# Kernel optimization log

Measured on AMD Instinct MI355X. Metric: run time of the kernel, lower is better.

## Reference

```python
import jax, jax.numpy as jnp
import numpy as np
import math

N_HEADS = 16


def setup_inputs() -> dict:
    key = jax.random.key(0)
    ks = jax.random.split(key, 5)
    B, S, E = 2, 2048, 1024
    scale = 1.0 / math.sqrt(E)
    return {
        "x": jax.random.normal(ks[0], (B, S, E), dtype=jnp.float32),
        "w_in": jax.random.normal(ks[1], (3 * E, E), dtype=jnp.float32) * scale,
        "b_in": jax.random.normal(ks[2], (3 * E,), dtype=jnp.float32) * 0.01,
        "w_out": jax.random.normal(ks[3], (E, E), dtype=jnp.float32) * scale,
        "b_out": jax.random.normal(ks[4], (E,), dtype=jnp.float32) * 0.01,
    }


def reference(x, w_in, b_in, w_out, b_out):
    B, S, E = x.shape
    H = N_HEADS
    d = E // H
    # fused QKV projection: [B,S,3E]
    qkv = x @ w_in.T + b_in
    q, k, v = jnp.split(qkv, 3, axis=-1)
    # [B,S,E] -> [B,H,S,d]
    q = q.reshape(B, S, H, d).transpose(0, 2, 1, 3)
    k = k.reshape(B, S, H, d).transpose(0, 2, 1, 3)
    v = v.reshape(B, S, H, d).transpose(0, 2, 1, 3)
    # scores [B,H,S,S], scaled by 1/sqrt(d_head) (no causal mask: casual_mask=False)
    scores = jnp.einsum("bhqd,bhkd->bhqk", q, k) / jnp.sqrt(jnp.float32(d)).astype(x.dtype)
    w = jax.nn.softmax(scores, axis=-1)
    # attention output [B,H,S,d] -> [B,S,E]
    out = jnp.einsum("bhqk,bhkd->bhqd", w, v)
    out = out.transpose(0, 2, 1, 3).reshape(B, S, E)
    return out @ w_out.T + b_out
```

## Files before the change

### kernel.cpp

```cpp
#include <hip/hip_runtime.h>
#include <cstdint>


typedef __bf16 bf16x8 __attribute__((ext_vector_type(8)));
typedef short s16x4 __attribute__((ext_vector_type(4)));
typedef float f32x4 __attribute__((ext_vector_type(4)));

__device__ __forceinline__ unsigned short f32_to_bf16_rne(float f) {
    unsigned int u = __builtin_bit_cast(unsigned int, f);
    u += 0x7FFF + ((u >> 16) & 1);
    return (unsigned short)(u >> 16);
}

__device__ __forceinline__ unsigned int pack_bf16_trunc(float a, float b) {
    unsigned int ua = __builtin_bit_cast(unsigned int, a);
    unsigned int ub = __builtin_bit_cast(unsigned int, b);
    return __builtin_amdgcn_perm(ub, ua, 0x07060302u);
}

__device__ __forceinline__ void gload16(const void* g, void* l) {
    __builtin_amdgcn_global_load_lds(
        (const __attribute__((address_space(1))) unsigned int*)g,
        (__attribute__((address_space(3))) unsigned int*)l, 16, 0, 0);
}

__global__ void cvt_all(const float* __restrict__ x, const float* __restrict__ wi,
                        const float* __restrict__ wo, unsigned short* __restrict__ xb,
                        unsigned short* __restrict__ wib, unsigned short* __restrict__ wob) {
    int i = blockIdx.x * blockDim.x + threadIdx.x;
    const float* src; unsigned short* dst; int off;
    if (i < 1048576)            { src = x;  dst = xb;  off = i; }
    else if (i < 1048576 + 786432) { src = wi; dst = wib; off = i - 1048576; }
    else                        { src = wo; dst = wob; off = i - (1048576 + 786432); }
    float4 v = ((const float4*)src)[off];
    ushort4 o;
    o.x = f32_to_bf16_rne(v.x); o.y = f32_to_bf16_rne(v.y);
    o.z = f32_to_bf16_rne(v.z); o.w = f32_to_bf16_rne(v.w);
    ((ushort4*)dst)[off] = o;
}

__launch_bounds__(256)
__global__ void gemm_qkv(const unsigned short* __restrict__ X,
                         const unsigned short* __restrict__ W,
                         const float* __restrict__ bias,
                         unsigned short* __restrict__ Qp,
                         unsigned short* __restrict__ Kp,
                         unsigned short* __restrict__ Vt) {
    __shared__ __align__(16) unsigned short As[128 * 64];
    __shared__ __align__(16) unsigned short Bs[128 * 64];
    const int t = threadIdx.x;
    const int w = t >> 6, lane = t & 63, quad = lane >> 4, l16 = lane & 15;
    const int wm = (w >> 1) * 64, wn = (w & 1) * 64;
    const int m0 = blockIdx.y * 128, n0 = blockIdx.x * 128;

    f32x4 acc[4][4] = {};

    for (int kt = 0; kt < 1024; kt += 64) {
        __syncthreads();
#pragma unroll
        for (int i = 0; i < 4; ++i) {
            int c = t + 256 * i;
            int r = c >> 3, cc = (c & 7) * 8;
            gload16(&X[(m0 + r) * 1024 + kt + cc], &As[c * 8]);
            gload16(&W[(n0 + r) * 1024 + kt + cc], &Bs[c * 8]);
        }
        __syncthreads();
#pragma unroll
        for (int ks = 0; ks < 2; ++ks) {
            bf16x8 af[4], bw[4];
#pragma unroll
            for (int mi = 0; mi < 4; ++mi)
                af[mi] = *(const bf16x8*)&As[(wm + mi * 16 + l16) * 64 + ks * 32 + quad * 8];
#pragma unroll
            for (int ni = 0; ni < 4; ++ni)
                bw[ni] = *(const bf16x8*)&Bs[(wn + ni * 16 + l16) * 64 + ks * 32 + quad * 8];
#pragma unroll
            for (int mi = 0; mi < 4; ++mi)
#pragma unroll
                for (int ni = 0; ni < 4; ++ni)
                    acc[mi][ni] = __builtin_amdgcn_mfma_f32_16x16x32_bf16(af[mi], bw[ni], acc[mi][ni], 0, 0, 0);
        }
    }

    const float QSCALE = 0.125f * 1.44269504089f;
#pragma unroll
    for (int mi = 0; mi < 4; ++mi) {
#pragma unroll
        for (int ni = 0; ni < 4; ++ni) {
            int col = n0 + wn + ni * 16 + l16;
            float bv = bias[col];
            int which = col >> 10;
            int hc = col & 1023;
            int h = hc >> 6, d = hc & 63;
            int row0 = m0 + wm + mi * 16 + quad * 4;
            int b = row0 >> 11, s0 = row0 & 2047;
            int bh = b * 16 + h;
            if (which == 2) {
                ushort4 pk;
                pk.x = f32_to_bf16_rne(acc[mi][ni][0] + bv);
                pk.y = f32_to_bf16_rne(acc[mi][ni][1] + bv);
                pk.z = f32_to_bf16_rne(acc[mi][ni][2] + bv);
                pk.w = f32_to_bf16_rne(acc[mi][ni][3] + bv);
                *(ushort4*)&Vt[(bh * 64 + d) * 2048 + s0] = pk;
            } else if (which == 0) {
#pragma unroll
                for (int r = 0; r < 4; ++r)
                    Qp[(bh * 2048 + s0 + r) * 64 + d] =
                        f32_to_bf16_rne((acc[mi][ni][r] + bv) * QSCALE);
            } else {
#pragma unroll
                for (int r = 0; r < 4; ++r)
                    Kp[(bh * 2048 + s0 + r) * 64 + d] = f32_to_bf16_rne(acc[mi][ni][r] + bv);
            }
        }
    }
}

__launch_bounds__(128, 2)
__global__ void attn(const unsigned short* __restrict__ Qp, const unsigned short* __restrict__ Kp,
                     const unsigned short* __restrict__ Vt, unsigned short* __restrict__ A2) {
    __shared__ __align__(16) unsigned short Ks[2][64 * 64];
    __shared__ __align__(16) unsigned short Vs[2][64 * 64];
    const int t = threadIdx.x, w = t >> 6, lane = t & 63, quad = lane >> 4, l16 = lane & 15;
    const int bh = blockIdx.x;
    const int qb = blockIdx.y;
    const unsigned short* Qh = Qp + bh * (2048 * 64);
    const unsigned short* Kh = Kp + bh * (2048 * 64);
    const unsigned short* Vh = Vt + bh * (64 * 2048);

    bf16x8 qf[2][2];
#pragma unroll
    for (int nq = 0; nq < 2; ++nq)
#pragma unroll
        for (int ks = 0; ks < 2; ++ks) {
            int row = qb * 64 + w * 32 + nq * 16 + l16;
            qf[nq][ks] = *(const bf16x8*)&Qh[row * 64 + ks * 32 + quad * 8];
        }

    f32x4 o_acc[4][2] = {};
    float l_lane[2] = {0.f, 0.f};

#pragma unroll
    for (int i = 0; i < 4; ++i) {
        int c = t + 128 * i;
        int r = c >> 3, sc = ((c & 7) ^ (r & 7)) << 3;
        gload16(&Kh[r * 64 + sc], &Ks[0][c * 8]);
        gload16(&Vh[r * 2048 + sc], &Vs[0][c * 8]);
    }

    int cur = 0;
    for (int it = 0; it < 32; ++it) {
        __syncthreads();
        if (it != 31) {
            int ktn = (it + 1) * 64;
#pragma unroll
            for (int i = 0; i < 4; ++i) {
                int c = t + 128 * i;
                int r = c >> 3, sc = ((c & 7) ^ (r & 7)) << 3;
                gload16(&Kh[(ktn + r) * 64 + sc], &Ks[cur ^ 1][c * 8]);
                gload16(&Vh[r * 2048 + ktn + sc], &Vs[cur ^ 1][c * 8]);
            }
        }
        const unsigned short* Kc = Ks[cur];
        const unsigned short* Vc = Vs[cur];

        f32x4 s_acc[4][2] = {};
#pragma unroll
        for (int ks = 0; ks < 2; ++ks)
#pragma unroll
            for (int mi = 0; mi < 4; ++mi) {
                bf16x8 kf = *(const bf16x8*)&Kc[(mi * 16 + l16) * 64 +
                                                (((ks * 4 + quad) ^ (l16 & 7)) << 3)];
#pragma unroll
                for (int nq = 0; nq < 2; ++nq)
                    s_acc[mi][nq] = __builtin_amdgcn_mfma_f32_16x16x32_bf16(kf, qf[nq][ks], s_acc[mi][nq], 0, 0, 0);
            }

        s16x4 bq[4][2];
#pragma unroll
        for (int nq = 0; nq < 2; ++nq) {
            float rsum = 0.f;
#pragma unroll
            for (int mi = 0; mi < 4; ++mi) {
                float p0 = __builtin_amdgcn_exp2f(s_acc[mi][nq][0]);
                float p1 = __builtin_amdgcn_exp2f(s_acc[mi][nq][1]);
                float p2 = __builtin_amdgcn_exp2f(s_acc[mi][nq][2]);
                float p3 = __builtin_amdgcn_exp2f(s_acc[mi][nq][3]);
                rsum += (p0 + p1) + (p2 + p3);
                uint2 pk;
                pk.x = pack_bf16_trunc(p0, p1);
                pk.y = pack_bf16_trunc(p2, p3);
                bq[mi][nq] = __builtin_bit_cast(s16x4, pk);
            }
            l_lane[nq] += rsum;
        }

#pragma unroll
        for (int dm = 0; dm < 4; ++dm)
#pragma unroll
            for (int kt4 = 0; kt4 < 4; ++kt4) {
                int ch = (kt4 * 2 + (quad >> 1)) ^ (l16 & 7);
                s16x4 av = __builtin_bit_cast(s16x4,
                    *(const uint2*)&Vc[(dm * 16 + l16) * 64 + (ch << 3) + (quad & 1) * 4]);
#pragma unroll
                for (int nq = 0; nq < 2; ++nq)
                    o_acc[dm][nq] = __builtin_amdgcn_mfma_f32_16x16x16bf16_1k(av, bq[kt4][nq], o_acc[dm][nq], 0, 0, 0);
            }
        cur ^= 1;
    }

    const int b = bh >> 4, h = bh & 15;
#pragma unroll
    for (int nq = 0; nq < 2; ++nq) {
        float l = l_lane[nq];
        l += __shfl_xor(l, 16);
        l += __shfl_xor(l, 32);
        float rl = 1.0f / l;
        int s = qb * 64 + w * 32 + nq * 16 + l16;
        int tok = b * 2048 + s;
#pragma unroll
        for (int dm = 0; dm < 4; ++dm) {
            ushort4 o;
            o.x = f32_to_bf16_rne(o_acc[dm][nq][0] * rl);
            o.y = f32_to_bf16_rne(o_acc[dm][nq][1] * rl);
            o.z = f32_to_bf16_rne(o_acc[dm][nq][2] * rl);
            o.w = f32_to_bf16_rne(o_acc[dm][nq][3] * rl);
            *(ushort4*)&A2[tok * 1024 + h * 64 + dm * 16 + quad * 4] = o;
        }
    }
}

__launch_bounds__(256)
__global__ void gemm_out_k(const unsigned short* __restrict__ A, const unsigned short* __restrict__ W,
                           const float* __restrict__ bias, float* __restrict__ out) {
    __shared__ __align__(16) unsigned short As[128 * 64];
    __shared__ __align__(16) unsigned short Bs[64 * 64];
    const int t = threadIdx.x;
    const int w = t >> 6, lane = t & 63, quad = lane >> 4, l16 = lane & 15;
    const int wm = (w >> 1) * 64, wn = (w & 1) * 32;
    const int m0 = blockIdx.y * 128, n0 = blockIdx.x * 64;

    f32x4 acc[4][2] = {};

    for (int kt = 0; kt < 1024; kt += 64) {
        __syncthreads();
#pragma unroll
        for (int i = 0; i < 4; ++i) {
            int c = t + 256 * i;
            int r = c >> 3, cc = (c & 7) * 8;
            gload16(&A[(m0 + r) * 1024 + kt + cc], &As[c * 8]);
        }
#pragma unroll
        for (int i = 0; i < 2; ++i) {
            int c = t + 256 * i;
            int r = c >> 3, cc = (c & 7) * 8;
            gload16(&W[(n0 + r) * 1024 + kt + cc], &Bs[c * 8]);
        }
        __syncthreads();
#pragma unroll
        for (int ks = 0; ks < 2; ++ks) {
            bf16x8 af[4], bw[2];
#pragma unroll
            for (int mi = 0; mi < 4; ++mi)
                af[mi] = *(const bf16x8*)&As[(wm + mi * 16 + l16) * 64 + ks * 32 + quad * 8];
#pragma unroll
            for (int ni = 0; ni < 2; ++ni)
                bw[ni] = *(const bf16x8*)&Bs[(wn + ni * 16 + l16) * 64 + ks * 32 + quad * 8];
#pragma unroll
            for (int mi = 0; mi < 4; ++mi)
#pragma unroll
                for (int ni = 0; ni < 2; ++ni)
                    acc[mi][ni] = __builtin_amdgcn_mfma_f32_16x16x32_bf16(af[mi], bw[ni], acc[mi][ni], 0, 0, 0);
        }
    }

#pragma unroll
    for (int mi = 0; mi < 4; ++mi)
#pragma unroll
        for (int ni = 0; ni < 2; ++ni) {
            int col = n0 + wn + ni * 16 + l16;
            float bv = bias[col];
#pragma unroll
            for (int r = 0; r < 4; ++r) {
                int row = m0 + wm + mi * 16 + quad * 4 + r;
                out[row * 1024 + col] = acc[mi][ni][r] + bv;
            }
        }
}

extern "C" void kernel_launch(void* const* d_in, const int* in_sizes, int n_in,
                              void* d_out, int out_size, void* d_ws, size_t ws_size,
                              hipStream_t stream) {
    const float* x     = (const float*)d_in[0];
    const float* w_in  = (const float*)d_in[1];
    const float* b_in  = (const float*)d_in[2];
    const float* w_out = (const float*)d_in[3];
    const float* b_out = (const float*)d_in[4];
    float* out = (float*)d_out;

    char* ws = (char*)d_ws;
    unsigned short* xb  = (unsigned short*)(ws);
    unsigned short* wib = (unsigned short*)(ws + 8388608);
    unsigned short* wob = (unsigned short*)(ws + 14680064);
    unsigned short* Qp  = (unsigned short*)(ws + 16777216);
    unsigned short* Kp  = (unsigned short*)(ws + 25165824);
    unsigned short* Vt  = (unsigned short*)(ws + 33554432);
    unsigned short* A2  = (unsigned short*)(ws + 41943040);

    cvt_all<<<8192, 256, 0, stream>>>(x, w_in, w_out, xb, wib, wob);
    gemm_qkv<<<dim3(24, 32), 256, 0, stream>>>(xb, wib, b_in, Qp, Kp, Vt);
    attn<<<dim3(32, 32), 128, 0, stream>>>(Qp, Kp, Vt, A2);
    gemm_out_k<<<dim3(16, 32), 256, 0, stream>>>(A2, wob, b_out, out);
}
```

Before: 214.6 us.

## Split attention KV tile across two wave pairs and reduce partial outputs in LDS

Doubles the attention block to 256 threads. Each pair of waves handles half of every 64-key tile, and the two partial output accumulators and row sums are combined through shared memory at the end. The aim is more waves per CU to hide MFMA, exp and load latency, and fewer registers per wave because the score and probability arrays are halved. The cost is an extra LDS reduction and two barriers in the epilogue. The softmax still uses no max subtraction, so splitting the sum is exact.

```diff
diff --git a/kernel.cpp b/kernel.cpp
--- a/kernel.cpp
+++ b/kernel.cpp
@@ -116,12 +116,15 @@
     }
 }
 
-__launch_bounds__(128, 2)
+__launch_bounds__(256, 4)
 __global__ void attn(const unsigned short* __restrict__ Qp, const unsigned short* __restrict__ Kp,
                      const unsigned short* __restrict__ Vt, unsigned short* __restrict__ A2) {
     __shared__ __align__(16) unsigned short Ks[2][64 * 64];
     __shared__ __align__(16) unsigned short Vs[2][64 * 64];
-    const int t = threadIdx.x, w = t >> 6, lane = t & 63, quad = lane >> 4, l16 = lane & 15;
+    const int t = threadIdx.x, lane = t & 63, quad = lane >> 4, l16 = lane & 15;
+    const int w = t >> 6;
+    const int wq = w & 1;
+    const int wk = w >> 1;
     const int bh = blockIdx.x;
     const int qb = blockIdx.y;
     const unsigned short* Qh = Qp + bh * (2048 * 64);
@@ -133,7 +136,7 @@
     for (int nq = 0; nq < 2; ++nq)
 #pragma unroll
         for (int ks = 0; ks < 2; ++ks) {
-            int row = qb * 64 + w * 32 + nq * 16 + l16;
+            int row = qb * 64 + wq * 32 + nq * 16 + l16;
             qf[nq][ks] = *(const bf16x8*)&Qh[row * 64 + ks * 32 + quad * 8];
         }
 
@@ -141,8 +144,8 @@
     float l_lane[2] = {0.f, 0.f};
 
 #pragma unroll
-    for (int i = 0; i < 4; ++i) {
-        int c = t + 128 * i;
+    for (int i = 0; i < 2; ++i) {
+        int c = t + 256 * i;
         int r = c >> 3, sc = ((c & 7) ^ (r & 7)) << 3;
         gload16(&Kh[r * 64 + sc], &Ks[0][c * 8]);
         gload16(&Vh[r * 2048 + sc], &Vs[0][c * 8]);
@@ -154,8 +157,8 @@
         if (it != 31) {
             int ktn = (it + 1) * 64;
 #pragma unroll
-            for (int i = 0; i < 4; ++i) {
-                int c = t + 128 * i;
+            for (int i = 0; i < 2; ++i) {
+                int c = t + 256 * i;
                 int r = c >> 3, sc = ((c & 7) ^ (r & 7)) << 3;
                 gload16(&Kh[(ktn + r) * 64 + sc], &Ks[cur ^ 1][c * 8]);
                 gload16(&Vh[r * 2048 + ktn + sc], &Vs[cur ^ 1][c * 8]);
@@ -164,24 +167,25 @@
         const unsigned short* Kc = Ks[cur];
         const unsigned short* Vc = Vs[cur];
 
-        f32x4 s_acc[4][2] = {};
+        f32x4 s_acc[2][2] = {};
 #pragma unroll
         for (int ks = 0; ks < 2; ++ks)
 #pragma unroll
-            for (int mi = 0; mi < 4; ++mi) {
-                bf16x8 kf = *(const bf16x8*)&Kc[(mi * 16 + l16) * 64 +
+            for (int mi = 0; mi < 2; ++mi) {
+                int row = wk * 32 + mi * 16 + l16;
+                bf16x8 kf = *(const bf16x8*)&Kc[row * 64 +
                                                 (((ks * 4 + quad) ^ (l16 & 7)) << 3)];
 #pragma unroll
                 for (int nq = 0; nq < 2; ++nq)
                     s_acc[mi][nq] = __builtin_amdgcn_mfma_f32_16x16x32_bf16(kf, qf[nq][ks], s_acc[mi][nq], 0, 0, 0);
             }
 
-        s16x4 bq[4][2];
+        s16x4 bq[2][2];
 #pragma unroll
         for (int nq = 0; nq < 2; ++nq) {
             float rsum = 0.f;
 #pragma unroll
-            for (int mi = 0; mi < 4; ++mi) {
+            for (int mi = 0; mi < 2; ++mi) {
                 float p0 = __builtin_amdgcn_exp2f(s_acc[mi][nq][0]);
                 float p1 = __builtin_amdgcn_exp2f(s_acc[mi][nq][1]);
                 float p2 = __builtin_amdgcn_exp2f(s_acc[mi][nq][2]);
@@ -198,8 +202,8 @@
 #pragma unroll
         for (int dm = 0; dm < 4; ++dm)
 #pragma unroll
-            for (int kt4 = 0; kt4 < 4; ++kt4) {
-                int ch = (kt4 * 2 + (quad >> 1)) ^ (l16 & 7);
+            for (int kt4 = 0; kt4 < 2; ++kt4) {
+                int ch = (wk * 4 + kt4 * 2 + (quad >> 1)) ^ (l16 & 7);
                 s16x4 av = __builtin_bit_cast(s16x4,
                     *(const uint2*)&Vc[(dm * 16 + l16) * 64 + (ch << 3) + (quad & 1) * 4]);
 #pragma unroll
@@ -209,23 +213,41 @@
         cur ^= 1;
     }
 
-    const int b = bh >> 4, h = bh & 15;
-#pragma unroll
-    for (int nq = 0; nq < 2; ++nq) {
-        float l = l_lane[nq];
-        l += __shfl_xor(l, 16);
-        l += __shfl_xor(l, 32);
-        float rl = 1.0f / l;
-        int s = qb * 64 + w * 32 + nq * 16 + l16;
-        int tok = b * 2048 + s;
-#pragma unroll
-        for (int dm = 0; dm < 4; ++dm) {
-            ushort4 o;
-            o.x = f32_to_bf16_rne(o_acc[dm][nq][0] * rl);
-            o.y = f32_to_bf16_rne(o_acc[dm][nq][1] * rl);
-            o.z = f32_to_bf16_rne(o_acc[dm][nq][2] * rl);
-            o.w = f32_to_bf16_rne(o_acc[dm][nq][3] * rl);
-            *(ushort4*)&A2[tok * 1024 + h * 64 + dm * 16 + quad * 4] = o;
+    __syncthreads();
+    float* fo = (float*)&Ks[0][0];
+    float* fl = (float*)&Vs[0][0];
+    if (wk == 1) {
+#pragma unroll
+        for (int nq = 0; nq < 2; ++nq) {
+#pragma unroll
+            for (int dm = 0; dm < 4; ++dm)
+                *(f32x4*)&fo[(wq * 32 + nq * 16 + l16) * 64 + dm * 16 + quad * 4] = o_acc[dm][nq];
+            fl[(wq * 2 + nq) * 64 + lane] = l_lane[nq];
+        }
+    }
+    __syncthreads();
+    if (wk == 0) {
+        const int b = bh >> 4, h = bh & 15;
+#pragma unroll
+        for (int nq = 0; nq < 2; ++nq) {
+#pragma unroll
+            for (int dm = 0; dm < 4; ++dm)
+                o_acc[dm][nq] += *(const f32x4*)&fo[(wq * 32 + nq * 16 + l16) * 64 + dm * 16 + quad * 4];
+            float l = l_lane[nq] + fl[(wq * 2 + nq) * 64 + lane];
+            l += __shfl_xor(l, 16);
+            l += __shfl_xor(l, 32);
+            float rl = 1.0f / l;
+            int s = qb * 64 + wq * 32 + nq * 16 + l16;
+            int tok = b * 2048 + s;
+#pragma unroll
+            for (int dm = 0; dm < 4; ++dm) {
+                ushort4 o;
+                o.x = f32_to_bf16_rne(o_acc[dm][nq][0] * rl);
+                o.y = f32_to_bf16_rne(o_acc[dm][nq][1] * rl);
+                o.z = f32_to_bf16_rne(o_acc[dm][nq][2] * rl);
+                o.w = f32_to_bf16_rne(o_acc[dm][nq][3] * rl);
+                *(ushort4*)&A2[tok * 1024 + h * 64 + dm * 16 + quad * 4] = o;
+            }
         }
     }
 }
@@ -309,6 +331,6 @@
 
     cvt_all<<<8192, 256, 0, stream>>>(x, w_in, w_out, xb, wib, wob);
     gemm_qkv<<<dim3(24, 32), 256, 0, stream>>>(xb, wib, b_in, Qp, Kp, Vt);
-    attn<<<dim3(32, 32), 128, 0, stream>>>(Qp, Kp, Vt, A2);
+    attn<<<dim3(32, 32), 256, 0, stream>>>(Qp, Kp, Vt, A2);
     gemm_out_k<<<dim3(16, 32), 256, 0, stream>>>(A2, wob, b_out, out);
 }
```

Measured after the change: 200.0 us. 1.07x faster.
